# Performance work log

Hardware: AMD Instinct MI355X
Metric: run time of the kernel (lower is better)

The kernel has to match this reference:

```python
import jax, jax.numpy as jnp
import numpy as np

SIGMA1 = 1.0        # RBF bandwidth for kernel1
DYADIC_ORDER = 1    # dyadic grid refinement
LAMBD = 1.0         # ridge regularizer
INPUT_SCALE = 0.1   # keep signature-kernel values in fp32 range


def rbf_gram(X, Y, sigma):
    # X: (N,S,D), Y: (M,T,D) -> (N,M,S,T), sigkernel RBFKernel: exp(-||x-y||^2 / sigma)
    x2 = jnp.sum(X * X, axis=-1)  # (N,S)
    y2 = jnp.sum(Y * Y, axis=-1)  # (M,T)
    xy = jnp.einsum('nsd,mtd->nmst', X, Y)
    d2 = x2[:, None, :, None] + y2[None, :, None, :] - 2.0 * xy
    return jnp.exp(-d2 / sigma)


def linear_gram(X, Y):
    # sigkernel LinearKernel: inner product Gram
    return jnp.einsum('nsd,mtd->nmst', X, Y)


def sig_kernel_gram(G, dyadic_order):
    """Solve the Goursat PDE for the signature kernel on a dyadic grid.

    G: (N,M,S,T) static-kernel Gram. Returns (N,M) signature-kernel Gram.
    Update (sigkernel explicit scheme):
      k[i+1,j+1] = (k[i+1,j] + k[i,j+1]) * (1 + inc/2 + inc^2/12)
                   - k[i,j] * (1 - inc^2/12)
    """
    N, M, S, T = G.shape
    # double increments of the static kernel
    inc = G[:, :, 1:, 1:] - G[:, :, 1:, :-1] - G[:, :, :-1, 1:] + G[:, :, :-1, :-1]
    f = 2 ** dyadic_order
    inc = jnp.repeat(jnp.repeat(inc, f, axis=2), f, axis=3) / float(f * f)
    B = N * M
    P, Q = (S - 1) * f, (T - 1) * f
    inc = inc.reshape(B, P, Q)
    C1 = 1.0 + 0.5 * inc + inc * inc * (1.0 / 12.0)
    C2 = 1.0 - inc * inc * (1.0 / 12.0)
    ones_b = jnp.ones((B,), G.dtype)

    def row_step(prev_row, coeffs):
        c1, c2 = coeffs  # (B,Q) each

        def col_step(left, v):
            c1j, c2j, pj, pjm1 = v  # each (B,)
            new = (left + pj) * c1j - pjm1 * c2j
            return new, new

        xs = (c1.T, c2.T, prev_row[:, 1:].T, prev_row[:, :-1].T)  # (Q,B)
        _, vals = jax.lax.scan(col_step, ones_b, xs)  # (Q,B)
        new_row = jnp.concatenate([ones_b[:, None], vals.T], axis=1)  # (B,Q+1)
        return new_row, None

    row0 = jnp.ones((B, Q + 1), G.dtype)
    last_row, _ = jax.lax.scan(row_step, row0, (jnp.moveaxis(C1, 1, 0), jnp.moveaxis(C2, 1, 0)))
    return last_row[:, -1].reshape(N, M)


def cmmd(x, y, z):
    N = x.shape[0]
    K = sig_kernel_gram(rbf_gram(x, x, SIGMA1), DYADIC_ORDER)
    L_gen = sig_kernel_gram(linear_gram(y, y), DYADIC_ORDER)
    L_true = sig_kernel_gram(linear_gram(z, z), DYADIC_ORDER)
    L_mix = sig_kernel_gram(linear_gram(y, z), DYADIC_ORDER)
    Ktildeinv = jnp.linalg.inv(K + jnp.eye(N, dtype=K.dtype) * LAMBD)
    A = K @ Ktildeinv  # shared left factor

    def tr(L):
        return jnp.trace(A @ (L @ Ktildeinv))

    return tr(L_gen) + tr(L_true) - 2.0 * tr(L_mix)


def setup_inputs() -> dict:
    key = jax.random.key(0)
    k1, k2, k3 = jax.random.split(key, 3)
    shape = (64, 33, 8)
    return {
        'x': jax.random.normal(k1, shape, dtype=jnp.float32) * INPUT_SCALE,
        'y': jax.random.normal(k2, shape, dtype=jnp.float32) * INPUT_SCALE,
        'z': jax.random.normal(k3, shape, dtype=jnp.float32) * INPUT_SCALE,
    }


def reference(x, y, z):
    return cmmd(x, y, z)
```

## Files before the change

kernel.cpp:

```cpp
#include <hip/hip_runtime.h>
#include <hip/hip_fp16.h>
#include <math.h>


#define SLEN 33

__device__ __forceinline__ float rl(float v, int lane) {
    return __int_as_float(__builtin_amdgcn_readlane(__float_as_int(v), lane));
}

__device__ __forceinline__ void pde_item(int g, int loc,
                                         const float* __restrict__ x,
                                         const float* __restrict__ y,
                                         const float* __restrict__ z,
                                         float* __restrict__ ws,
                                         float4 (*Xi4)[66],
                                         __half (*incH)[1024]) {
    const int lane = threadIdx.x & 63;
    const int h = lane >> 5;
    const int p = lane & 31;

    int pair = 2 * loc + h, gi, gj;
    if (g == 3) {
        gi = pair >> 6; gj = pair & 63;
    } else {
        float ff = sqrtf(8.0f * (float)pair + 1.0f);
        gi = (int)((ff - 1.0f) * 0.5f);
        while ((gi + 1) * (gi + 2) / 2 <= pair) ++gi;
        while (gi * (gi + 1) / 2 > pair) --gi;
        gj = pair - gi * (gi + 1) / 2;
    }

    const float* Ap = (g == 0) ? x : ((g == 2) ? z : y);
    const float* Bp = (g == 0) ? x : ((g == 1) ? y : z);
    const float4* As = (const float4*)(Ap + gi * (SLEN * 8));
    const float4* Bs = (const float4*)(Bp + gj * (SLEN * 8));

    for (int k = p; k < 66; k += 32) Xi4[h][k] = As[k];
    float4 b0 = Bs[2*p],   b1 = Bs[2*p+1];
    float4 b2 = Bs[2*p+2], b3 = Bs[2*p+3];
    __syncthreads();

    if (g == 0) {
        float nprev;
        {
            float4 a0 = Xi4[h][0], a1 = Xi4[h][1];
            float d0=a0.x-b0.x,d1=a0.y-b0.y,d2=a0.z-b0.z,d3=a0.w-b0.w;
            float d4=a1.x-b1.x,d5=a1.y-b1.y,d6=a1.z-b1.z,d7=a1.w-b1.w;
            float da = d0*d0+d1*d1+d2*d2+d3*d3+d4*d4+d5*d5+d6*d6+d7*d7;
            float e0=a0.x-b2.x,e1=a0.y-b2.y,e2=a0.z-b2.z,e3=a0.w-b2.w;
            float e4=a1.x-b3.x,e5=a1.y-b3.y,e6=a1.z-b3.z,e7=a1.w-b3.w;
            float db = e0*e0+e1*e1+e2*e2+e3*e3+e4*e4+e5*e5+e6*e6+e7*e7;
            nprev = __expf(-db) - __expf(-da);
        }
        for (int k = 1; k <= 32; ++k) {
            float4 a0 = Xi4[h][2*k], a1 = Xi4[h][2*k+1];
            float d0=a0.x-b0.x,d1=a0.y-b0.y,d2=a0.z-b0.z,d3=a0.w-b0.w;
            float d4=a1.x-b1.x,d5=a1.y-b1.y,d6=a1.z-b1.z,d7=a1.w-b1.w;
            float da = d0*d0+d1*d1+d2*d2+d3*d3+d4*d4+d5*d5+d6*d6+d7*d7;
            float e0=a0.x-b2.x,e1=a0.y-b2.y,e2=a0.z-b2.z,e3=a0.w-b2.w;
            float e4=a1.x-b3.x,e5=a1.y-b3.y,e6=a1.z-b3.z,e7=a1.w-b3.w;
            float db = e0*e0+e1*e1+e2*e2+e3*e3+e4*e4+e5*e5+e6*e6+e7*e7;
            float diffk = __expf(-db) - __expf(-da);
            incH[h][(k-1)*32 + p] = __float2half(0.25f * (diffk - nprev));
            nprev = diffk;
        }
    } else {
        float e0=b2.x-b0.x, e1=b2.y-b0.y, e2=b2.z-b0.z, e3=b2.w-b0.w;
        float e4=b3.x-b1.x, e5=b3.y-b1.y, e6=b3.z-b1.z, e7=b3.w-b1.w;
        float4 a0 = Xi4[h][0], a1 = Xi4[h][1];
        #pragma unroll 4
        for (int k = 0; k < 32; ++k) {
            float4 a2 = Xi4[h][2*k+2], a3 = Xi4[h][2*k+3];
            float acc = (a2.x-a0.x)*e0 + (a2.y-a0.y)*e1
                      + (a2.z-a0.z)*e2 + (a2.w-a0.w)*e3
                      + (a3.x-a1.x)*e4 + (a3.y-a1.y)*e5
                      + (a3.z-a1.z)*e6 + (a3.w-a1.w)*e7;
            incH[h][k*32 + p] = __float2half(0.25f * acc);
            a0 = a2; a1 = a3;
        }
    }
    __syncthreads();

    float c01 = 1.0f, c10 = 1.0f, c11 = 1.0f, dcarry = 1.0f;
    const bool isrow0 = (p == 0);
    const __half* incrow = &incH[h][p * 32];
    #pragma unroll 4
    for (int m = 0; m < 63; ++m) {
        float nb10 = __shfl_up(c10, 1);
        float nb11 = __shfl_up(c11, 1);
        int t = m - p;
        float incv = __half2float(incrow[t & 31]);
        float n0 = isrow0 ? 1.0f : nb10;
        float n1 = isrow0 ? 1.0f : nb11;
        bool t0 = (t == 0);
        float w0 = t0 ? 1.0f : c01;
        float w1 = t0 ? 1.0f : c11;
        float d  = t0 ? 1.0f : dcarry;
        float i2 = incv * incv * (1.0f / 12.0f);
        float C1 = 1.0f + 0.5f * incv + i2;
        float C2 = 1.0f - i2;
        float v00 = (w0  + n0 ) * C1 - d   * C2;
        float v01 = (v00 + n1 ) * C1 - n0  * C2;
        float v10 = (v00 + w1 ) * C1 - w0  * C2;
        float v11 = (v10 + v01) * C1 - v00 * C2;
        c01 = v01; c10 = v10; c11 = v11;
        dcarry = n1;
    }

    if (p == 31) {
        float* dst = ws + g * 4096;
        dst[gi * 64 + gj] = c11;
        if (g != 3) dst[gj * 64 + gi] = c11;
    }
}

__global__ __launch_bounds__(64, 5)
void pdeK_kernel(const float* __restrict__ x, const float* __restrict__ y,
                 const float* __restrict__ z, float* __restrict__ ws) {
    __shared__ float4 XiS[2][66];
    __shared__ __half incS[2][1024];
    pde_item(0, blockIdx.x, x, y, z, ws, XiS, incS);
}

__global__ __launch_bounds__(512, 4)
void pdeL_gj_kernel(const float* __restrict__ x, const float* __restrict__ y,
                    const float* __restrict__ z, float* __restrict__ ws,
                    float* __restrict__ out) {
    __shared__ float4 XiS[16][66];
    __shared__ __half incS[16][1024];
    __shared__ float prow[2][2][64];

    const int b   = blockIdx.x;
    const int tid = threadIdx.x;
    const int wv  = tid >> 6;

    if (b == 0) {
        const int c = tid & 63, w = wv;
        const float* K = ws;
        float* Kinv = ws + 16384;
        float m[8];
        #pragma unroll
        for (int i = 0; i < 8; ++i) {
            int r = w * 8 + i;
            m[i] = K[r * 64 + c] + ((r == c) ? 1.0f : 0.0f);
        }
        #pragma unroll 1
        for (int it = 0; it < 8; ++it) {
            #pragma unroll
            for (int j = 0; j < 4; ++j) {
                const int p0 = 8 * it + 2 * j, p1 = p0 + 1;
                const int i0 = 2 * j, i1 = i0 + 1;
                const int buf = j & 1;
                if (w == it) {
                    float x0 = m[i0], x1 = m[i1];
                    float a  = rl(x0, p0), bq = rl(x0, p1);
                    float cq = rl(x1, p0), dq = rl(x1, p1);
                    float dinv = 1.0f / (a * dq - bq * cq);
                    float P00 =  dq * dinv, P01 = -bq * dinv;
                    float P10 = -cq * dinv, P11 =  a  * dinv;
                    float sp0 = P00 * x0 + P01 * x1;
                    float sp1 = P10 * x0 + P11 * x1;
                    sp0 = (c == p0) ? P00 : ((c == p1) ? P01 : sp0);
                    sp1 = (c == p0) ? P10 : ((c == p1) ? P11 : sp1);
                    m[i0] = sp0; m[i1] = sp1;
                    prow[buf][0][c] = sp0;
                    prow[buf][1][c] = sp1;
                }
                __syncthreads();
                float s0  = prow[buf][0][c],  s1  = prow[buf][1][c];
                float q00 = prow[buf][0][p0], q01 = prow[buf][0][p1];
                float q10 = prow[buf][1][p0], q11 = prow[buf][1][p1];
                #pragma unroll
                for (int i = 0; i < 8; ++i) {
                    bool pivotRow = (w == it) && (i == i0 || i == i1);
                    float f0 = rl(m[i], p0);
                    float f1 = rl(m[i], p1);
                    float nv = m[i] - f0 * s0 - f1 * s1;
                    float wb0 = -(f0 * q00 + f1 * q10);
                    float wb1 = -(f0 * q01 + f1 * q11);
                    nv = (c == p0) ? wb0 : ((c == p1) ? wb1 : nv);
                    if (!pivotRow) m[i] = nv;
                }
            }
        }
        #pragma unroll
        for (int i = 0; i < 8; ++i)
            Kinv[(w * 8 + i) * 64 + c] = m[i];
        if (tid == 0) out[0] = 0.0f;
    } else {
        int item = (b - 1) * 8 + wv;
        int g, loc;
        if (item < 1040)      { g = 1; loc = item; }
        else if (item < 2080) { g = 2; loc = item - 1040; }
        else                  { g = 3; loc = item - 2080; }
        pde_item(g, loc, x, y, z, ws, &XiS[2 * wv], &incS[2 * wv]);
    }
}

__global__ __launch_bounds__(64)
void trace_kernel(const float* __restrict__ ws, float* __restrict__ out) {
    const int i    = blockIdx.x;
    const int lane = threadIdx.x;
    const float* Lg   = ws + 4096;
    const float* Lt   = ws + 8192;
    const float* Lm   = ws + 12288;
    const float* Kinv = ws + 16384;

    float u = Kinv[i * 64 + lane];
    float acc = 0.0f;
    #pragma unroll 8
    for (int k = 0; k < 64; ++k)
        acc = fmaf(__shfl(u, k), Kinv[k * 64 + lane], acc);
    float wv = u - acc;

    float lc = Lg[lane * 64 + i] + Lt[lane * 64 + i] - 2.0f * Lm[lane * 64 + i];
    float local = wv * lc;
    #pragma unroll
    for (int off = 32; off > 0; off >>= 1)
        local += __shfl_down(local, off);
    if (lane == 0) atomicAdd(out, local);
}

extern "C" void kernel_launch(void* const* d_in, const int* in_sizes, int n_in,
                              void* d_out, int out_size, void* d_ws, size_t ws_size,
                              hipStream_t stream) {
    const float* x = (const float*)d_in[0];
    const float* y = (const float*)d_in[1];
    const float* z = (const float*)d_in[2];
    float* out = (float*)d_out;
    float* ws  = (float*)d_ws;

    pdeK_kernel<<<1040, 64, 0, stream>>>(x, y, z, ws);
    pdeL_gj_kernel<<<517, 512, 0, stream>>>(x, y, z, ws, out);
    trace_kernel<<<64, 64, 0, stream>>>(ws, out);
}
```

Measured before the change: 98.53 us.

## Fuse K-gram PDE into main kernel with atomic counter handoff to inverse block

Merges the separate K-gram PDE launch into the main kernel, so 1040 K items run as extra waves alongside the L items. Block 0 spin-waits on a global atomic counter until every K item has finished, then computes the matrix inverse. Per-item __syncthreads are replaced with a wave-local LDS wait, since each item lives within one wavefront. This removes one kernel launch and the serialization between the K PDE and the L PDE. In exchange it relies on block 0 being resident while the others run, and block 0 may stall its CU while it spins.

```diff
diff --git a/kernel.cpp b/kernel.cpp
--- a/kernel.cpp
+++ b/kernel.cpp
@@ -4,9 +4,16 @@
 
 
 #define SLEN 33
+#define K_ITEMS 1040
+
+__device__ int g_kcnt = 0;
 
 __device__ __forceinline__ float rl(float v, int lane) {
     return __int_as_float(__builtin_amdgcn_readlane(__float_as_int(v), lane));
+}
+
+__device__ __forceinline__ void wave_lds_sync() {
+    asm volatile("s_waitcnt lgkmcnt(0)" ::: "memory");
 }
 
 __device__ __forceinline__ void pde_item(int g, int loc,
@@ -39,7 +46,7 @@
     for (int k = p; k < 66; k += 32) Xi4[h][k] = As[k];
     float4 b0 = Bs[2*p],   b1 = Bs[2*p+1];
     float4 b2 = Bs[2*p+2], b3 = Bs[2*p+3];
-    __syncthreads();
+    wave_lds_sync();
 
     if (g == 0) {
         float nprev;
@@ -80,7 +87,7 @@
             a0 = a2; a1 = a3;
         }
     }
-    __syncthreads();
+    wave_lds_sync();
 
     float c01 = 1.0f, c10 = 1.0f, c11 = 1.0f, dcarry = 1.0f;
     const bool isrow0 = (p == 0);
@@ -113,20 +120,16 @@
         dst[gi * 64 + gj] = c11;
         if (g != 3) dst[gj * 64 + gi] = c11;
     }
-}
-
-__global__ __launch_bounds__(64, 5)
-void pdeK_kernel(const float* __restrict__ x, const float* __restrict__ y,
-                 const float* __restrict__ z, float* __restrict__ ws) {
-    __shared__ float4 XiS[2][66];
-    __shared__ __half incS[2][1024];
-    pde_item(0, blockIdx.x, x, y, z, ws, XiS, incS);
+    if (g == 0) {
+        __threadfence();
+        if (lane == 0) atomicAdd(&g_kcnt, 1);
+    }
 }
 
 __global__ __launch_bounds__(512, 4)
-void pdeL_gj_kernel(const float* __restrict__ x, const float* __restrict__ y,
-                    const float* __restrict__ z, float* __restrict__ ws,
-                    float* __restrict__ out) {
+void fused_kernel(const float* __restrict__ x, const float* __restrict__ y,
+                  const float* __restrict__ z, float* __restrict__ ws,
+                  float* __restrict__ out) {
     __shared__ float4 XiS[16][66];
     __shared__ __half incS[16][1024];
     __shared__ float prow[2][2][64];
@@ -136,6 +139,17 @@
     const int wv  = tid >> 6;
 
     if (b == 0) {
+        if (tid == 0) {
+            out[0] = 0.0f;
+            while (__hip_atomic_load(&g_kcnt, __ATOMIC_RELAXED,
+                                     __HIP_MEMORY_SCOPE_AGENT) < K_ITEMS)
+                __builtin_amdgcn_s_sleep(2);
+            __hip_atomic_store(&g_kcnt, 0, __ATOMIC_RELAXED,
+                               __HIP_MEMORY_SCOPE_AGENT);
+        }
+        __syncthreads();
+        __threadfence();
+
         const int c = tid & 63, w = wv;
         const float* K = ws;
         float* Kinv = ws + 16384;
@@ -187,13 +201,13 @@
         #pragma unroll
         for (int i = 0; i < 8; ++i)
             Kinv[(w * 8 + i) * 64 + c] = m[i];
-        if (tid == 0) out[0] = 0.0f;
     } else {
         int item = (b - 1) * 8 + wv;
         int g, loc;
-        if (item < 1040)      { g = 1; loc = item; }
-        else if (item < 2080) { g = 2; loc = item - 1040; }
-        else                  { g = 3; loc = item - 2080; }
+        if (item < 1040)      { g = 0; loc = item; }
+        else if (item < 2080) { g = 1; loc = item - 1040; }
+        else if (item < 3120) { g = 2; loc = item - 2080; }
+        else                  { g = 3; loc = item - 3120; }
         pde_item(g, loc, x, y, z, ws, &XiS[2 * wv], &incS[2 * wv]);
     }
 }
@@ -231,7 +245,6 @@
     float* out = (float*)d_out;
     float* ws  = (float*)d_ws;
 
-    pdeK_kernel<<<1040, 64, 0, stream>>>(x, y, z, ws);
-    pdeL_gj_kernel<<<517, 512, 0, stream>>>(x, y, z, ws, out);
+    fused_kernel<<<647, 512, 0, stream>>>(x, y, z, ws, out);
     trace_kernel<<<64, 64, 0, stream>>>(ws, out);
 }
```

New measurement: 124.3 us. 1.26x slower.
